# Kernel tuning notes

Measured on AMD Instinct MI355X. Metric: run time of the kernel, lower is better.

The kernel has to match this reference:

```python
import jax, jax.numpy as jnp
import numpy as np

B, S, L = 32, 512, 64
START, STOP, PAD = 61, 62, 63
NEG = -10000.0


def setup_inputs() -> dict:
    key = jax.random.key(0)
    k1, k2, k3, k4 = jax.random.split(key, 4)
    encoder_scores = jax.random.normal(k1, (B, S, L), dtype=jnp.float32)
    transition = jax.random.normal(k2, (L, L), dtype=jnp.float32)
    # constrained transitions, as in __init__
    transition = (transition.at[:, START].set(NEG)
                            .at[STOP, :].set(NEG)
                            .at[:, PAD].set(NEG)
                            .at[PAD, :].set(NEG))
    word_seq_lens = jax.random.randint(k3, (B,), S // 2, S + 1)  # in [S/2, S]
    tags = jax.random.randint(k4, (B, S), 0, START)  # valid non-special labels
    mask = jnp.arange(S)[None, :] < word_seq_lens[:, None]
    return {"encoder_scores": encoder_scores, "transition": transition,
            "word_seq_lens": word_seq_lens, "tags": tags, "mask": mask}


def reference(encoder_scores, transition, word_seq_lens, tags, mask):
    # all_scores[b,s,i,j] = transition[i,j] + encoder_scores[b,s,j]  (B,S,L,L)
    all_scores = transition[None, None, :, :] + encoder_scores[:, :, None, :]

    # ---- forward algorithm (partition function) ----
    alpha0 = all_scores[:, 0, START, :]  # (B,L)

    def step(a_prev, s_t):  # a_prev (B,L), s_t (B,L,L)
        a = jax.nn.logsumexp(a_prev[:, :, None] + s_t, axis=1)
        return a, a

    _, alphas_rest = jax.lax.scan(step, alpha0,
                                  jnp.swapaxes(all_scores[:, 1:], 0, 1))
    alphas = jnp.concatenate([alpha0[:, None, :],
                              jnp.swapaxes(alphas_rest, 0, 1)], axis=1)  # (B,S,L)
    last_alpha = jnp.take_along_axis(
        alphas, (word_seq_lens - 1)[:, None, None], axis=1)[:, 0, :]  # (B,L)
    last_alpha = last_alpha + transition[:, STOP][None, :]
    unlabeled = jax.nn.logsumexp(last_alpha, axis=1)  # (B,)

    # ---- gold-sequence score ----
    # cur[b,s,i] = all_scores[b,s,i,tags[b,s]]
    cur = jnp.take_along_axis(all_scores, tags[:, :, None, None], axis=3)[..., 0]  # (B,S,L)
    mid = jnp.take_along_axis(cur[:, 1:, :], tags[:, :-1, None], axis=2)[..., 0]  # (B,S-1)
    begin = cur[:, 0, START]  # (B,)
    end_ids = jnp.take_along_axis(tags, (word_seq_lens - 1)[:, None], axis=1)[:, 0]
    end_sc = transition[end_ids, STOP]  # (B,)
    labeled = begin + end_sc + jnp.sum(mid * mask[:, 1:].astype(mid.dtype), axis=1)
    return unlabeled, labeled
```

## Files before the change

kernel.cpp:

```cpp
#include <hip/hip_runtime.h>
#include <hip/hip_bf16.h>

#define BB 32
#define SS 512
#define LL 64
#define TSTART 61
#define TSTOP 62
#define NSEG 16
#define SEGLEN 32
#define QPAD 68
#define AFPAD 36

typedef short short8 __attribute__((ext_vector_type(8)));
typedef float floatx4 __attribute__((ext_vector_type(4)));

union S8 { int i[4]; short8 v; };

__device__ inline int pack_bf16(float a, float b) {
    __hip_bfloat162 h = __float22bfloat162_rn(make_float2(a, b));
    int r;
    __builtin_memcpy(&r, &h, 4);
    return r;
}

__global__ __launch_bounds__(256) void crf_seg_kernel(
    const float* __restrict__ enc, const float* __restrict__ Tr,
    const int* __restrict__ lens, const int* __restrict__ tags,
    float* __restrict__ wsQ, float* __restrict__ wsS,
    float* __restrict__ out)
{
    const int blk = blockIdx.x;
    const int tid = threadIdx.x;
    if (blk >= BB * NSEG) {
        const int b = blk - BB * NSEG;
        const int len = lens[b];
        const int* tg = tags + b * SS;
        const float* eb = enc + b * (SS * LL);
        float acc = 0.f;
        for (int t = 1 + tid; t < len; t += 256) {
            int curt = tg[t], prevt = tg[t - 1];
            acc += Tr[prevt * LL + curt] + eb[t * LL + curt];
        }
        #pragma unroll
        for (int off = 32; off; off >>= 1) acc += __shfl_xor(acc, off);
        __shared__ float red[4];
        if ((tid & 63) == 0) red[tid >> 6] = acc;
        __syncthreads();
        if (tid == 0) {
            float tot = (red[0] + red[1]) + (red[2] + red[3]);
            int t0 = tg[0], te = tg[len - 1];
            tot += Tr[TSTART * LL + t0] + eb[t0];
            tot += Tr[te * LL + TSTOP];
            out[BB + b] = tot;
        }
        return;
    }

    const int lane = tid & 63;
    const int g = tid >> 6;
    const int xr = blk & 7;
    const int pk = blk >> 3;
    const int b = xr + 8 * (pk >> 4);
    const int s = pk & 15;
    const int len = lens[b];
    const int q = lane >> 4;
    const int lcol = lane & 15;
    const float* eb = enc + b * (SS * LL);
    const int tlo = SEGLEN * s + 1;
    const int Teff = min(max(len - tlo, 0), SEGLEN);

    float* qdst = wsQ + (size_t)(b * NSEG + s) * 4096;

    if (Teff <= 0) {
        #pragma unroll
        for (int c4 = 0; c4 < 4; ++c4) {
            int c0 = 16 * g + 4 * c4;
            float4 v;
            v.x = (c0 + 0 == lane) ? 1.f : 0.f;
            v.y = (c0 + 1 == lane) ? 1.f : 0.f;
            v.z = (c0 + 2 == lane) ? 1.f : 0.f;
            v.w = (c0 + 3 == lane) ? 1.f : 0.f;
            *(float4*)(qdst + lane * 64 + c0) = v;
        }
        if (lane == 0) wsS[(b * NSEG + s) * 4 + g] = 0.f;
        return;
    }

    __shared__ __align__(16) float QT_all[4][16 * QPAD];
    __shared__ __align__(16) float W32[32 * 64];
    __shared__ __align__(16) int   AF[64 * AFPAD];

    float* QT = QT_all[g];

    {
        const int al = tid & 63, amt = tid >> 6;
        const int aq = al >> 4, alc = al & 15;
        #pragma unroll
        for (int c2 = 0; c2 < 2; ++c2) {
            float av[8];
            #pragma unroll
            for (int idx = 0; idx < 8; ++idx)
                av[idx] = __expf(Tr[(32 * c2 + 8 * aq + idx) * LL + 16 * amt + alc]) * 0.0078125f;
            int4 w;
            w.x = pack_bf16(av[0], av[1]);
            w.y = pack_bf16(av[2], av[3]);
            w.z = pack_bf16(av[4], av[5]);
            w.w = pack_bf16(av[6], av[7]);
            *(int4*)(AF + al * AFPAD + (amt * 2 + c2) * 4) = w;
        }
    }

    {
        const float* trow = Tr + (16 * g + lcol) * LL;
        #pragma unroll
        for (int u = 0; u < 4; ++u) {
            float4 tv = *(const float4*)(trow + 16 * q + 4 * u);
            float4 ev;
            ev.x = __expf(tv.x) * 0.0078125f;
            ev.y = __expf(tv.y) * 0.0078125f;
            ev.z = __expf(tv.z) * 0.0078125f;
            ev.w = __expf(tv.w) * 0.0078125f;
            *(float4*)(QT + lcol * QPAD + 16 * q + 4 * u) = ev;
        }
    }

    const int r0 = tid >> 6;
    const int colt = tid & 63;
    float ecur[2], enxt[2];
    ecur[0] = eb[min(tlo + r0,     SS - 1) * LL + colt];
    ecur[1] = eb[min(tlo + r0 + 4, SS - 1) * LL + colt];
    enxt[0] = eb[min(tlo + 8 + r0,     SS - 1) * LL + colt];
    enxt[1] = eb[min(tlo + 8 + r0 + 4, SS - 1) * LL + colt];

    short8 Afr[4][2];
    float lg = 0.0f;

    for (int cc = 0; cc < 4; ++cc) {
        W32[(8 * cc + r0) * 64 + colt]     = __expf(ecur[0]);
        W32[(8 * cc + 4 + r0) * 64 + colt] = __expf(ecur[1]);
        float epre[2];
        epre[0] = eb[min(tlo + 8 * (cc + 2) + r0,     SS - 1) * LL + colt];
        epre[1] = eb[min(tlo + 8 * (cc + 2) + r0 + 4, SS - 1) * LL + colt];

        __syncthreads();

        if (cc == 0) {
            #pragma unroll
            for (int mt = 0; mt < 4; ++mt)
                #pragma unroll
                for (int c2 = 0; c2 < 2; ++c2) {
                    S8 u;
                    *(int4*)u.i = *(const int4*)(AF + lane * AFPAD + (mt * 2 + c2) * 4);
                    Afr[mt][c2] = u.v;
                }
        }

        #pragma unroll
        for (int k = 0; k < 8; ++k) {
            const int i = 8 * cc + k + 2;
            if (i <= Teff) {
                const int wloc = 8 * cc + k;
                float4 qv[2][2], wv[2][2];
                #pragma unroll
                for (int c2 = 0; c2 < 2; ++c2)
                    #pragma unroll
                    for (int h = 0; h < 2; ++h) {
                        qv[c2][h] = *(const float4*)(QT + lcol * QPAD + 32 * c2 + 8 * q + 4 * h);
                        wv[c2][h] = *(const float4*)(W32 + wloc * 64 + 32 * c2 + 8 * q + 4 * h);
                    }
                short8 Bfr[2];
                #pragma unroll
                for (int c2 = 0; c2 < 2; ++c2) {
                    float bv[8];
                    bv[0] = qv[c2][0].x * wv[c2][0].x;  bv[1] = qv[c2][0].y * wv[c2][0].y;
                    bv[2] = qv[c2][0].z * wv[c2][0].z;  bv[3] = qv[c2][0].w * wv[c2][0].w;
                    bv[4] = qv[c2][1].x * wv[c2][1].x;  bv[5] = qv[c2][1].y * wv[c2][1].y;
                    bv[6] = qv[c2][1].z * wv[c2][1].z;  bv[7] = qv[c2][1].w * wv[c2][1].w;
                    S8 u;
                    u.i[0] = pack_bf16(bv[0], bv[1]);
                    u.i[1] = pack_bf16(bv[2], bv[3]);
                    u.i[2] = pack_bf16(bv[4], bv[5]);
                    u.i[3] = pack_bf16(bv[6], bv[7]);
                    Bfr[c2] = u.v;
                }
                float ov[4][4];
                #pragma unroll
                for (int mt = 0; mt < 4; ++mt) {
                    floatx4 z = {0.f, 0.f, 0.f, 0.f};
                    z = __builtin_amdgcn_mfma_f32_16x16x32_bf16(Afr[mt][0], Bfr[0], z, 0, 0, 0);
                    z = __builtin_amdgcn_mfma_f32_16x16x32_bf16(Afr[mt][1], Bfr[1], z, 0, 0, 0);
                    ov[mt][0] = z[0]; ov[mt][1] = z[1]; ov[mt][2] = z[2]; ov[mt][3] = z[3];
                }
                if (k == 7) {
                    float mx = ov[0][0];
                    #pragma unroll
                    for (int mt = 0; mt < 4; ++mt)
                        #pragma unroll
                        for (int r = 0; r < 4; ++r) mx = fmaxf(mx, ov[mt][r]);
                    #pragma unroll
                    for (int off = 32; off; off >>= 1) mx = fmaxf(mx, __shfl_xor(mx, off));
                    lg += __logf(mx);
                    float rmx = 1.0f / mx;
                    #pragma unroll
                    for (int mt = 0; mt < 4; ++mt)
                        #pragma unroll
                        for (int r = 0; r < 4; ++r) ov[mt][r] *= rmx;
                }
                #pragma unroll
                for (int mt = 0; mt < 4; ++mt) {
                    float4 sv = make_float4(ov[mt][0], ov[mt][1], ov[mt][2], ov[mt][3]);
                    *(float4*)(QT + lcol * QPAD + 16 * mt + 4 * q) = sv;
                }
            }
        }
        ecur[0] = enxt[0]; ecur[1] = enxt[1];
        enxt[0] = epre[0]; enxt[1] = epre[1];
    }

    {
        const float wj = W32[(Teff - 1) * 64 + lane];
        #pragma unroll
        for (int c4 = 0; c4 < 4; ++c4) {
            float4 o;
            o.x = QT[(4 * c4 + 0) * QPAD + lane] * wj;
            o.y = QT[(4 * c4 + 1) * QPAD + lane] * wj;
            o.z = QT[(4 * c4 + 2) * QPAD + lane] * wj;
            o.w = QT[(4 * c4 + 3) * QPAD + lane] * wj;
            *(float4*)(qdst + lane * 64 + 16 * g + 4 * c4) = o;
        }
    }
    if (lane == 0) wsS[(b * NSEG + s) * 4 + g] = lg;
}

__global__ __launch_bounds__(64) void crf_combine_kernel(
    const float* __restrict__ enc, const float* __restrict__ Tr,
    const int* __restrict__ lens,
    const float* __restrict__ wsQ, const float* __restrict__ wsS,
    float* __restrict__ out)
{
    const int b = blockIdx.x;
    const int j = threadIdx.x;
    const int len = lens[b];
    const float* qb = wsQ + (size_t)b * NSEG * 4096;

    float alpha0 = Tr[TSTART * LL + j] + enc[b * (SS * LL) + j];
    float m = alpha0;
    #pragma unroll
    for (int off = 32; off; off >>= 1) m = fmaxf(m, __shfl_xor(m, off));
    float a = __expf(alpha0 - m);
    float logscale = m;

    float myscale = wsS[b * (NSEG * 4) + j];

    float A[64], Bv[64];
    #pragma unroll
    for (int i = 0; i < 16; ++i) {
        float4 t = *(const float4*)(qb + j * 64 + 4 * i);
        A[4 * i + 0] = t.x; A[4 * i + 1] = t.y; A[4 * i + 2] = t.z; A[4 * i + 3] = t.w;
    }

    auto step = [&](int s, float (&cur)[64]) {
        float l0 = __shfl(myscale, 4 * s + 0);
        float l1 = __shfl(myscale, 4 * s + 1);
        float l2 = __shfl(myscale, 4 * s + 2);
        float l3 = __shfl(myscale, 4 * s + 3);
        float lmax = fmaxf(fmaxf(l0, l1), fmaxf(l2, l3));
        int grp = j >> 4;
        float lgg = (grp == 0) ? l0 : (grp == 1) ? l1 : (grp == 2) ? l2 : l3;
        float at = a * __expf(lgg - lmax);
        int ai = __float_as_int(at);
        float s0 = 0.f, s1 = 0.f, s2 = 0.f, s3 = 0.f;
        #pragma unroll
        for (int c = 0; c < 16; ++c) {
            s0 = fmaf(__int_as_float(__builtin_amdgcn_readlane(ai, 4 * c + 0)), cur[4 * c + 0], s0);
            s1 = fmaf(__int_as_float(__builtin_amdgcn_readlane(ai, 4 * c + 1)), cur[4 * c + 1], s1);
            s2 = fmaf(__int_as_float(__builtin_amdgcn_readlane(ai, 4 * c + 2)), cur[4 * c + 2], s2);
            s3 = fmaf(__int_as_float(__builtin_amdgcn_readlane(ai, 4 * c + 3)), cur[4 * c + 3], s3);
        }
        float an = ((s0 + s1) + (s2 + s3));
        float mx = an;
        #pragma unroll
        for (int off = 32; off; off >>= 1) mx = fmaxf(mx, __shfl_xor(mx, off));
        a = an * (1.0f / mx);
        logscale += lmax + __logf(mx);
    };

    for (int s = 0; s < 16; s += 2) {
        const float* q1 = qb + (size_t)min(s + 1, NSEG - 1) * 4096;
        #pragma unroll
        for (int i = 0; i < 16; ++i) {
            float4 t = *(const float4*)(q1 + j * 64 + 4 * i);
            Bv[4 * i + 0] = t.x; Bv[4 * i + 1] = t.y; Bv[4 * i + 2] = t.z; Bv[4 * i + 3] = t.w;
        }
        step(s, A);
        const float* q2 = qb + (size_t)min(s + 2, NSEG - 1) * 4096;
        #pragma unroll
        for (int i = 0; i < 16; ++i) {
            float4 t = *(const float4*)(q2 + j * 64 + 4 * i);
            A[4 * i + 0] = t.x; A[4 * i + 1] = t.y; A[4 * i + 2] = t.z; A[4 * i + 3] = t.w;
        }
        step(s + 1, Bv);
    }

    float f = a * __expf(Tr[j * LL + TSTOP]);
    float ssum = f;
    #pragma unroll
    for (int off = 32; off; off >>= 1) ssum += __shfl_xor(ssum, off);
    if (j == 0) {
        const float LN2x7 = 7.0f * 0.69314718055994530942f;
        out[b] = logscale + (float)(len - 1) * LN2x7 + __logf(ssum);
    }
}

__global__ __launch_bounds__(256) void crf_kernel_fb(
    const float* __restrict__ enc, const float* __restrict__ Tr,
    const int* __restrict__ lens, const int* __restrict__ tags,
    float* __restrict__ out)
{
    if (blockIdx.x < BB) {
        const int tid = threadIdx.x;
        if (tid >= 64) return;
        const int b = blockIdx.x;
        const int j = tid;
        const int len = lens[b];
        const float* eb = enc + b * (SS * LL);
        float Ecol[LL];
        #pragma unroll
        for (int i = 0; i < LL; ++i) Ecol[i] = __expf(Tr[i * LL + j]) * 0.0078125f;
        float alpha0 = Tr[TSTART * LL + j] + eb[j];
        float m = alpha0;
        #pragma unroll
        for (int off = 32; off; off >>= 1) m = fmaxf(m, __shfl_xor(m, off));
        float a = __expf(alpha0 - m);
        float logscale = m;
        float ecur[4], enext[4];
        #pragma unroll
        for (int k = 0; k < 4; ++k) ecur[k] = eb[k * LL + j];
        #pragma unroll
        for (int k = 0; k < 4; ++k) enext[k] = eb[(4 + k) * LL + j];
        const int nchunk = (len + 3) >> 2;
        for (int c = 0; c < nchunk; ++c) {
            const int cpre = (c + 2 < 128) ? (c + 2) : 127;
            float efar[4];
            #pragma unroll
            for (int k = 0; k < 4; ++k) efar[k] = eb[(4 * cpre + k) * LL + j];
            #pragma unroll
            for (int k = 0; k < 4; ++k) {
                const int t = 4 * c + k;
                if (t >= 1 && t < len) {
                    const float w = __expf(ecur[k]);
                    const int ai = __float_as_int(a);
                    float s0 = 0.f, s1 = 0.f, s2 = 0.f, s3 = 0.f;
                    #pragma unroll
                    for (int qq = 0; qq < 16; ++qq) {
                        s0 = fmaf(__int_as_float(__builtin_amdgcn_readlane(ai, 4 * qq + 0)), Ecol[4 * qq + 0], s0);
                        s1 = fmaf(__int_as_float(__builtin_amdgcn_readlane(ai, 4 * qq + 1)), Ecol[4 * qq + 1], s1);
                        s2 = fmaf(__int_as_float(__builtin_amdgcn_readlane(ai, 4 * qq + 2)), Ecol[4 * qq + 2], s2);
                        s3 = fmaf(__int_as_float(__builtin_amdgcn_readlane(ai, 4 * qq + 3)), Ecol[4 * qq + 3], s3);
                    }
                    a = ((s0 + s1) + (s2 + s3)) * w;
                    if ((t & 7) == 7) {
                        float mm = a;
                        #pragma unroll
                        for (int off = 32; off; off >>= 1) mm = fmaxf(mm, __shfl_xor(mm, off));
                        logscale += __logf(mm);
                        a = a * (1.0f / mm);
                    }
                }
            }
            #pragma unroll
            for (int k = 0; k < 4; ++k) { ecur[k] = enext[k]; enext[k] = efar[k]; }
        }
        float f = a * __expf(Tr[j * LL + TSTOP]);
        float ssum = f;
        #pragma unroll
        for (int off = 32; off; off >>= 1) ssum += __shfl_xor(ssum, off);
        if (j == 0) {
            const float LN2x7 = 7.0f * 0.69314718055994530942f;
            out[b] = logscale + (float)(len - 1) * LN2x7 + __logf(ssum);
        }
    } else {
        const int b = blockIdx.x - BB;
        const int tid = threadIdx.x;
        const int len = lens[b];
        const int* tg = tags + b * SS;
        const float* eb = enc + b * (SS * LL);
        float acc = 0.f;
        for (int t = 1 + tid; t < len; t += 256) {
            int curt = tg[t], prevt = tg[t - 1];
            acc += Tr[prevt * LL + curt] + eb[t * LL + curt];
        }
        #pragma unroll
        for (int off = 32; off; off >>= 1) acc += __shfl_xor(acc, off);
        __shared__ float red[4];
        if ((tid & 63) == 0) red[tid >> 6] = acc;
        __syncthreads();
        if (tid == 0) {
            float tot = (red[0] + red[1]) + (red[2] + red[3]);
            int t0 = tg[0], te = tg[len - 1];
            tot += Tr[TSTART * LL + t0] + eb[t0];
            tot += Tr[te * LL + TSTOP];
            out[BB + b] = tot;
        }
    }
}

extern "C" void kernel_launch(void* const* d_in, const int* in_sizes, int n_in,
                              void* d_out, int out_size, void* d_ws, size_t ws_size,
                              hipStream_t stream) {
    const float* enc  = (const float*)d_in[0];
    const float* Tr   = (const float*)d_in[1];
    const int*   lens = (const int*)d_in[2];
    const int*   tags = (const int*)d_in[3];
    float* out = (float*)d_out;

    const size_t needQ = (size_t)BB * NSEG * 4096 * sizeof(float);
    const size_t needS = (size_t)BB * NSEG * 4 * sizeof(float);
    if (ws_size >= needQ + needS) {
        float* wsQ = (float*)d_ws;
        float* wsS = (float*)((char*)d_ws + needQ);
        crf_seg_kernel<<<BB * NSEG + BB, 256, 0, stream>>>(enc, Tr, lens, tags, wsQ, wsS, out);
        crf_combine_kernel<<<BB, 64, 0, stream>>>(enc, Tr, lens, wsQ, wsS, out);
    } else {
        crf_kernel_fb<<<2 * BB, 256, 0, stream>>>(enc, Tr, lens, tags, out);
    }
}
```

Before: 96.34 us.

## Keep segment transfer state in registers and use 16x16x16 MFMA chaining

The segment kernel now keeps the running transfer matrix in registers as MFMA accumulator outputs. It no longer round-trips that matrix through a per-wave LDS tile, and it switches to 16x16x16 bf16 MFMAs whose output layout feeds the next step's B operand directly. All exp(emission) rows are precomputed into LDS up front with one barrier instead of per-chunk barriers. The next row is prefetched from LDS during compute. The combine kernel prefetches the next segment's scale shuffles and only renormalizes when values approach overflow or underflow, which removes a per-step wave max-reduction. The trade-offs are more MFMA instructions per step, strided scalar global stores for the output, and reliance on a range check for numerical safety.

```diff
diff --git a/kernel.cpp b/kernel.cpp
--- a/kernel.cpp
+++ b/kernel.cpp
@@ -8,13 +8,12 @@
 #define TSTOP 62
 #define NSEG 16
 #define SEGLEN 32
-#define QPAD 68
 #define AFPAD 36
 
-typedef short short8 __attribute__((ext_vector_type(8)));
+typedef short short4v __attribute__((ext_vector_type(4)));
 typedef float floatx4 __attribute__((ext_vector_type(4)));
 
-union S8 { int i[4]; short8 v; };
+union S4 { int i[2]; short4v v; };
 
 __device__ inline int pack_bf16(float a, float b) {
     __hip_bfloat162 h = __float22bfloat162_rn(make_float2(a, b));
@@ -86,148 +85,121 @@
         return;
     }
 
-    __shared__ __align__(16) float QT_all[4][16 * QPAD];
     __shared__ __align__(16) float W32[32 * 64];
     __shared__ __align__(16) int   AF[64 * AFPAD];
 
-    float* QT = QT_all[g];
-
     {
-        const int al = tid & 63, amt = tid >> 6;
+        const int colt = tid & 63, r8 = tid >> 6;
+        #pragma unroll
+        for (int jj = 0; jj < 8; ++jj) {
+            int row = r8 * 8 + jj;
+            W32[row * 64 + colt] = __expf(eb[min(tlo + row, SS - 1) * LL + colt]);
+        }
+    }
+
+    {
+        const int al = tid & 63, mtT = tid >> 6;
         const int aq = al >> 4, alc = al & 15;
         #pragma unroll
-        for (int c2 = 0; c2 < 2; ++c2) {
-            float av[8];
-            #pragma unroll
-            for (int idx = 0; idx < 8; ++idx)
-                av[idx] = __expf(Tr[(32 * c2 + 8 * aq + idx) * LL + 16 * amt + alc]) * 0.0078125f;
-            int4 w;
-            w.x = pack_bf16(av[0], av[1]);
-            w.y = pack_bf16(av[2], av[3]);
-            w.z = pack_bf16(av[4], av[5]);
-            w.w = pack_bf16(av[6], av[7]);
-            *(int4*)(AF + al * AFPAD + (amt * 2 + c2) * 4) = w;
-        }
-    }
-
+        for (int kc = 0; kc < 4; ++kc) {
+            float av[4];
+            #pragma unroll
+            for (int idx = 0; idx < 4; ++idx)
+                av[idx] = __expf(Tr[(16 * kc + 4 * aq + idx) * LL + 16 * mtT + alc]) * 0.0078125f;
+            AF[al * AFPAD + mtT * 8 + kc * 2 + 0] = pack_bf16(av[0], av[1]);
+            AF[al * AFPAD + mtT * 8 + kc * 2 + 1] = pack_bf16(av[2], av[3]);
+        }
+    }
+
+    float R[4][4];
     {
         const float* trow = Tr + (16 * g + lcol) * LL;
         #pragma unroll
-        for (int u = 0; u < 4; ++u) {
-            float4 tv = *(const float4*)(trow + 16 * q + 4 * u);
-            float4 ev;
-            ev.x = __expf(tv.x) * 0.0078125f;
-            ev.y = __expf(tv.y) * 0.0078125f;
-            ev.z = __expf(tv.z) * 0.0078125f;
-            ev.w = __expf(tv.w) * 0.0078125f;
-            *(float4*)(QT + lcol * QPAD + 16 * q + 4 * u) = ev;
-        }
-    }
-
-    const int r0 = tid >> 6;
-    const int colt = tid & 63;
-    float ecur[2], enxt[2];
-    ecur[0] = eb[min(tlo + r0,     SS - 1) * LL + colt];
-    ecur[1] = eb[min(tlo + r0 + 4, SS - 1) * LL + colt];
-    enxt[0] = eb[min(tlo + 8 + r0,     SS - 1) * LL + colt];
-    enxt[1] = eb[min(tlo + 8 + r0 + 4, SS - 1) * LL + colt];
-
-    short8 Afr[4][2];
+        for (int mt = 0; mt < 4; ++mt) {
+            float4 tv = *(const float4*)(trow + 16 * mt + 4 * q);
+            R[mt][0] = __expf(tv.x) * 0.0078125f;
+            R[mt][1] = __expf(tv.y) * 0.0078125f;
+            R[mt][2] = __expf(tv.z) * 0.0078125f;
+            R[mt][3] = __expf(tv.w) * 0.0078125f;
+        }
+    }
+
+    __syncthreads();
+
+    short4v Afr[4][4];
+    #pragma unroll
+    for (int mt = 0; mt < 4; ++mt)
+        #pragma unroll
+        for (int kc = 0; kc < 4; ++kc) {
+            S4 u;
+            u.i[0] = AF[lane * AFPAD + mt * 8 + kc * 2 + 0];
+            u.i[1] = AF[lane * AFPAD + mt * 8 + kc * 2 + 1];
+            Afr[mt][kc] = u.v;
+        }
+
+    float4 wreg[4];
+    #pragma unroll
+    for (int mt = 0; mt < 4; ++mt)
+        wreg[mt] = *(const float4*)(W32 + 16 * mt + 4 * q);
+
     float lg = 0.0f;
-
-    for (int cc = 0; cc < 4; ++cc) {
-        W32[(8 * cc + r0) * 64 + colt]     = __expf(ecur[0]);
-        W32[(8 * cc + 4 + r0) * 64 + colt] = __expf(ecur[1]);
-        float epre[2];
-        epre[0] = eb[min(tlo + 8 * (cc + 2) + r0,     SS - 1) * LL + colt];
-        epre[1] = eb[min(tlo + 8 * (cc + 2) + r0 + 4, SS - 1) * LL + colt];
-
-        __syncthreads();
-
-        if (cc == 0) {
-            #pragma unroll
-            for (int mt = 0; mt < 4; ++mt)
+    const int nst = Teff - 1;
+
+    #pragma unroll
+    for (int k = 0; k < 32; ++k) {
+        if (k < nst) {
+            short4v Bfr[4];
+            #pragma unroll
+            for (int kc = 0; kc < 4; ++kc) {
+                float s0 = R[kc][0] * wreg[kc].x, s1 = R[kc][1] * wreg[kc].y;
+                float s2 = R[kc][2] * wreg[kc].z, s3 = R[kc][3] * wreg[kc].w;
+                S4 u;
+                u.i[0] = pack_bf16(s0, s1);
+                u.i[1] = pack_bf16(s2, s3);
+                Bfr[kc] = u.v;
+            }
+            float4 wnx[4];
+            {
+                const int krow = min(k + 1, 31);
                 #pragma unroll
-                for (int c2 = 0; c2 < 2; ++c2) {
-                    S8 u;
-                    *(int4*)u.i = *(const int4*)(AF + lane * AFPAD + (mt * 2 + c2) * 4);
-                    Afr[mt][c2] = u.v;
-                }
-        }
-
-        #pragma unroll
-        for (int k = 0; k < 8; ++k) {
-            const int i = 8 * cc + k + 2;
-            if (i <= Teff) {
-                const int wloc = 8 * cc + k;
-                float4 qv[2][2], wv[2][2];
+                for (int mt = 0; mt < 4; ++mt)
+                    wnx[mt] = *(const float4*)(W32 + krow * 64 + 16 * mt + 4 * q);
+            }
+            #pragma unroll
+            for (int mt = 0; mt < 4; ++mt) {
+                floatx4 z = {0.f, 0.f, 0.f, 0.f};
                 #pragma unroll
-                for (int c2 = 0; c2 < 2; ++c2)
+                for (int kc = 0; kc < 4; ++kc)
+                    z = __builtin_amdgcn_mfma_f32_16x16x16bf16_1k(Afr[mt][kc], Bfr[kc], z, 0, 0, 0);
+                R[mt][0] = z[0]; R[mt][1] = z[1]; R[mt][2] = z[2]; R[mt][3] = z[3];
+            }
+            if ((k & 7) == 7) {
+                float mx = R[0][0];
+                #pragma unroll
+                for (int mt = 0; mt < 4; ++mt)
                     #pragma unroll
-                    for (int h = 0; h < 2; ++h) {
-                        qv[c2][h] = *(const float4*)(QT + lcol * QPAD + 32 * c2 + 8 * q + 4 * h);
-                        wv[c2][h] = *(const float4*)(W32 + wloc * 64 + 32 * c2 + 8 * q + 4 * h);
-                    }
-                short8 Bfr[2];
+                    for (int r = 0; r < 4; ++r) mx = fmaxf(mx, R[mt][r]);
                 #pragma unroll
-                for (int c2 = 0; c2 < 2; ++c2) {
-                    float bv[8];
-                    bv[0] = qv[c2][0].x * wv[c2][0].x;  bv[1] = qv[c2][0].y * wv[c2][0].y;
-                    bv[2] = qv[c2][0].z * wv[c2][0].z;  bv[3] = qv[c2][0].w * wv[c2][0].w;
-                    bv[4] = qv[c2][1].x * wv[c2][1].x;  bv[5] = qv[c2][1].y * wv[c2][1].y;
-                    bv[6] = qv[c2][1].z * wv[c2][1].z;  bv[7] = qv[c2][1].w * wv[c2][1].w;
-                    S8 u;
-                    u.i[0] = pack_bf16(bv[0], bv[1]);
-                    u.i[1] = pack_bf16(bv[2], bv[3]);
-                    u.i[2] = pack_bf16(bv[4], bv[5]);
-                    u.i[3] = pack_bf16(bv[6], bv[7]);
-                    Bfr[c2] = u.v;
-                }
-                float ov[4][4];
+                for (int off = 32; off; off >>= 1) mx = fmaxf(mx, __shfl_xor(mx, off));
+                lg += __logf(mx);
+                float rmx = 1.0f / mx;
                 #pragma unroll
-                for (int mt = 0; mt < 4; ++mt) {
-                    floatx4 z = {0.f, 0.f, 0.f, 0.f};
-                    z = __builtin_amdgcn_mfma_f32_16x16x32_bf16(Afr[mt][0], Bfr[0], z, 0, 0, 0);
-                    z = __builtin_amdgcn_mfma_f32_16x16x32_bf16(Afr[mt][1], Bfr[1], z, 0, 0, 0);
-                    ov[mt][0] = z[0]; ov[mt][1] = z[1]; ov[mt][2] = z[2]; ov[mt][3] = z[3];
-                }
-                if (k == 7) {
-                    float mx = ov[0][0];
+                for (int mt = 0; mt < 4; ++mt)
                     #pragma unroll
-                    for (int mt = 0; mt < 4; ++mt)
-                        #pragma unroll
-                        for (int r = 0; r < 4; ++r) mx = fmaxf(mx, ov[mt][r]);
-                    #pragma unroll
-                    for (int off = 32; off; off >>= 1) mx = fmaxf(mx, __shfl_xor(mx, off));
-                    lg += __logf(mx);
-                    float rmx = 1.0f / mx;
-                    #pragma unroll
-                    for (int mt = 0; mt < 4; ++mt)
-                        #pragma unroll
-                        for (int r = 0; r < 4; ++r) ov[mt][r] *= rmx;
-                }
-                #pragma unroll
-                for (int mt = 0; mt < 4; ++mt) {
-                    float4 sv = make_float4(ov[mt][0], ov[mt][1], ov[mt][2], ov[mt][3]);
-                    *(float4*)(QT + lcol * QPAD + 16 * mt + 4 * q) = sv;
-                }
+                    for (int r = 0; r < 4; ++r) R[mt][r] *= rmx;
             }
-        }
-        ecur[0] = enxt[0]; ecur[1] = enxt[1];
-        enxt[0] = epre[0]; enxt[1] = epre[1];
-    }
-
-    {
-        const float wj = W32[(Teff - 1) * 64 + lane];
-        #pragma unroll
-        for (int c4 = 0; c4 < 4; ++c4) {
-            float4 o;
-            o.x = QT[(4 * c4 + 0) * QPAD + lane] * wj;
-            o.y = QT[(4 * c4 + 1) * QPAD + lane] * wj;
-            o.z = QT[(4 * c4 + 2) * QPAD + lane] * wj;
-            o.w = QT[(4 * c4 + 3) * QPAD + lane] * wj;
-            *(float4*)(qdst + lane * 64 + 16 * g + 4 * c4) = o;
-        }
+            #pragma unroll
+            for (int mt = 0; mt < 4; ++mt) wreg[mt] = wnx[mt];
+        }
+    }
+
+    #pragma unroll
+    for (int mt = 0; mt < 4; ++mt) {
+        float4 wl = *(const float4*)(W32 + (Teff - 1) * 64 + 16 * mt + 4 * q);
+        qdst[(16 * mt + 4 * q + 0) * 64 + 16 * g + lcol] = R[mt][0] * wl.x;
+        qdst[(16 * mt + 4 * q + 1) * 64 + 16 * g + lcol] = R[mt][1] * wl.y;
+        qdst[(16 * mt + 4 * q + 2) * 64 + 16 * g + lcol] = R[mt][2] * wl.z;
+        qdst[(16 * mt + 4 * q + 3) * 64 + 16 * g + lcol] = R[mt][3] * wl.w;
     }
     if (lane == 0) wsS[(b * NSEG + s) * 4 + g] = lg;
 }
@@ -259,14 +231,16 @@
         A[4 * i + 0] = t.x; A[4 * i + 1] = t.y; A[4 * i + 2] = t.z; A[4 * i + 3] = t.w;
     }
 
+    float l0 = __shfl(myscale, 0), l1 = __shfl(myscale, 1);
+    float l2 = __shfl(myscale, 2), l3 = __shfl(myscale, 3);
+
     auto step = [&](int s, float (&cur)[64]) {
-        float l0 = __shfl(myscale, 4 * s + 0);
-        float l1 = __shfl(myscale, 4 * s + 1);
-        float l2 = __shfl(myscale, 4 * s + 2);
-        float l3 = __shfl(myscale, 4 * s + 3);
         float lmax = fmaxf(fmaxf(l0, l1), fmaxf(l2, l3));
         int grp = j >> 4;
         float lgg = (grp == 0) ? l0 : (grp == 1) ? l1 : (grp == 2) ? l2 : l3;
+        int sn = (s + 1 < NSEG) ? s + 1 : NSEG - 1;
+        float n0 = __shfl(myscale, 4 * sn + 0), n1 = __shfl(myscale, 4 * sn + 1);
+        float n2 = __shfl(myscale, 4 * sn + 2), n3 = __shfl(myscale, 4 * sn + 3);
         float at = a * __expf(lgg - lmax);
         int ai = __float_as_int(at);
         float s0 = 0.f, s1 = 0.f, s2 = 0.f, s3 = 0.f;
@@ -278,11 +252,17 @@
             s3 = fmaf(__int_as_float(__builtin_amdgcn_readlane(ai, 4 * c + 3)), cur[4 * c + 3], s3);
         }
         float an = ((s0 + s1) + (s2 + s3));
-        float mx = an;
-        #pragma unroll
-        for (int off = 32; off; off >>= 1) mx = fmaxf(mx, __shfl_xor(mx, off));
-        a = an * (1.0f / mx);
-        logscale += lmax + __logf(mx);
+        logscale += lmax;
+        if (__any(an > 1e28f) || __all(an < 1e-28f)) {
+            float mx = an;
+            #pragma unroll
+            for (int off = 32; off; off >>= 1) mx = fmaxf(mx, __shfl_xor(mx, off));
+            a = an * (1.0f / mx);
+            logscale += __logf(mx);
+        } else {
+            a = an;
+        }
+        l0 = n0; l1 = n1; l2 = n2; l3 = n3;
     };
 
     for (int s = 0; s < 16; s += 2) {
```

After: 89.32 us. 1.08x faster.
